# Kernel tuning notes

Measured on AMD Instinct MI355X. Metric: run time of the kernel, lower is better.

The kernel has to match this reference:

```python
import jax, jax.numpy as jnp
import numpy as np

FILTERS = 64
HIDDEN = 128
T_PRED = 24
DILATIONS = (1, 2, 4, 8, 16, 32)
N_DIL = len(DILATIONS)
FEAT = 15
B = 1024
L_ENC = 168


def setup_inputs() -> dict:
    key = jax.random.key(0)
    ks = jax.random.split(key, 16)
    s = 0.05
    d_in = 1 + FEAT  # prev_output (1) concat current feature
    inp = {
        "decoder_features": jax.random.normal(ks[0], (B, T_PRED, FEAT), jnp.float32),
        "decoder_init_input": jax.random.normal(ks[1], (B, 1), jnp.float32),
        "encoder_states": jax.random.normal(ks[2], (N_DIL, B, L_ENC, FILTERS), jnp.float32),
        # dense_1: d_in -> filters (tanh)
        "W1": jax.random.normal(ks[3], (d_in, FILTERS), jnp.float32) * s,
        "b1": jnp.zeros((FILTERS,), jnp.float32),
        # dense_2: filters -> 2*filters (bias)
        "W2": jax.random.normal(ks[4], (FILTERS, 2 * FILTERS), jnp.float32) * s,
        "b2": jnp.zeros((2 * FILTERS,), jnp.float32),
        # dense_3: filters -> 2*filters (no bias)
        "W3": jax.random.normal(ks[5], (FILTERS, 2 * FILTERS), jnp.float32) * s,
        # dense_4: filters -> 2*filters (bias)
        "W4": jax.random.normal(ks[6], (FILTERS, 2 * FILTERS), jnp.float32) * s,
        "b4": jnp.zeros((2 * FILTERS,), jnp.float32),
        # dense_5: n_dil*filters -> hidden (relu)
        "W5": jax.random.normal(ks[7], (N_DIL * FILTERS, HIDDEN), jnp.float32) * s,
        "b5": jnp.zeros((HIDDEN,), jnp.float32),
        # dense_6: hidden -> 1
        "W6": jax.random.normal(ks[8], (HIDDEN, 1), jnp.float32) * s,
        "b6": jnp.zeros((1,), jnp.float32),
    }
    return inp


def _decode(decoder_features, decoder_init_input, encoder_states,
            W1, b1, W2, b2, W3, W4, b4, W5, b5, W6, b6):
    L = encoder_states.shape[2]
    # 'appended' holds the inputs written back into each dilation's state
    # (the growing-concat part of encoder_states in the original loop).
    appended0 = jnp.zeros((N_DIL, decoder_features.shape[0], T_PRED, FILTERS),
                          dtype=decoder_features.dtype)

    def step(carry, t):
        prev, appended = carry
        cur = jnp.concatenate([prev, decoder_features[:, t, :]], axis=1)  # [B, 1+FEAT]
        inputs = jnp.tanh(cur @ W1 + b1)  # [B, F]
        skips_list = []
        for i, d in enumerate(DILATIONS):
            # grown-state read index is (L + t) - d; if t >= d it lands in the
            # appended region (step t-d), otherwise in the original encoder state.
            idx_app = jnp.clip(t - d, 0, T_PRED - 1)
            idx_orig = jnp.clip(L + t - d, 0, L - 1)
            st_app = jax.lax.dynamic_index_in_dim(appended[i], idx_app, axis=1, keepdims=False)
            st_orig = jax.lax.dynamic_index_in_dim(encoder_states[i], idx_orig, axis=1, keepdims=False)
            state = jnp.where(t >= d, st_app, st_orig)  # [B, F]
            dilated = state @ W2 + b2 + inputs @ W3  # [B, 2F]
            conv_filter, conv_gate = dilated[:, :FILTERS], dilated[:, FILTERS:]
            gated = jnp.tanh(conv_filter) * jax.nn.sigmoid(conv_gate)
            out = gated @ W4 + b4  # [B, 2F]
            skips, residuals = out[:, :FILTERS], out[:, FILTERS:]
            inputs = inputs + residuals
            appended = appended.at[i, :, t, :].set(inputs)
            skips_list.append(skips)
        skip = jax.nn.relu(jnp.concatenate(skips_list, axis=1))  # [B, N_DIL*F]
        h = jax.nn.relu(skip @ W5 + b5)
        y = h @ W6 + b6  # [B, 1]
        return (y, appended), y

    (_, _), ys = jax.lax.scan(step, (decoder_init_input, appended0),
                              jnp.arange(T_PRED))
    return jnp.transpose(ys, (1, 0, 2))  # [B, T, 1]


def reference(decoder_features, decoder_init_input, encoder_states,
              W1, b1, W2, b2, W3, W4, b4, W5, b5, W6, b6):
    return _decode(decoder_features, decoder_init_input, encoder_states,
                   W1, b1, W2, b2, W3, W4, b4, W5, b5, W6, b6)
```

## Files before the change

kernel.cpp:

```cpp
#include <hip/hip_runtime.h>

typedef _Float16 h16;
typedef _Float16 half8 __attribute__((ext_vector_type(8)));
typedef float floatx4 __attribute__((ext_vector_type(4)));

#define B_TOT 1024
#define T_STEPS 24
#define F 64
#define C2 128
#define FEAT 15
#define L_ENC 168
#define HID 128
#define R 16
#define BLK 256
#define FP 72
#define W5_WS_ELEMS (12*8*64*8)

__device__ __forceinline__ floatx4 mfma16(half8 a, half8 b, floatx4 c) {
  return __builtin_amdgcn_mfma_f32_16x16x32_f16(a, b, c, 0, 0, 0);
}

__global__ void prep_w5(const float* __restrict__ gW5, h16* __restrict__ wsW5) {
  int t = blockIdx.x * 256 + threadIdx.x;
  if (t >= 12 * 8 * 64) return;
  int lane = t & 63, nt = (t >> 6) & 7, ktg = t >> 9;
  int n  = nt * 16 + (lane & 15);
  int kb = ktg * 32 + (lane >> 4) * 8;
  half8 v;
  #pragma unroll
  for (int j = 0; j < 8; ++j) v[j] = (h16)gW5[(size_t)(kb + j) * C2 + n];
  *(half8*)&wsW5[(size_t)t * 8] = v;
}

__global__ __launch_bounds__(BLK) void decoder_v6(
    const float* __restrict__ dec_feat,
    const float* __restrict__ dec_init,
    const float* __restrict__ enc,
    const float* __restrict__ gW1, const float* __restrict__ gb1,
    const float* __restrict__ gW2, const float* __restrict__ gb2,
    const float* __restrict__ gW3,
    const float* __restrict__ gW4, const float* __restrict__ gb4,
    const h16*  __restrict__ wsW5, const float* __restrict__ gb5,
    const float* __restrict__ gW6, const float* __restrict__ gb6,
    float* __restrict__ out)
{
  __shared__ alignas(16) h16 sW2B[8][2][64][8];
  __shared__ alignas(16) h16 sW3B[8][2][64][8];
  __shared__ alignas(16) h16 sW4B[8][2][64][8];
  __shared__ alignas(16) h16 sW1B[4][64][8];
  __shared__ alignas(16) h16 ringL[31][R][FP];
  __shared__ alignas(16) h16 xH[R][FP];
  __shared__ alignas(16) float x32[R][F];
  __shared__ alignas(16) h16 gatedH[R][FP];
  __shared__ alignas(16) h16 skipH[R][FP];
  __shared__ alignas(16) h16 curH[R][40];
  __shared__ float sb1[F], sb2[C2], sb4[C2], sb5[HID], sW6v[HID];
  __shared__ float ypart[4][R];
  __shared__ float sb6;

  const int tid  = threadIdx.x;
  const int w    = tid >> 6;
  const int lane = tid & 63;
  const int m16  = lane & 15;
  const int q    = lane >> 4;
  const int q8   = q * 8;
  const int b0   = blockIdx.x * R;

  #pragma unroll
  for (int it = 0; it < 4; ++it) {
    int tsk = tid + BLK * it;
    int ln = tsk & 63, kt = (tsk >> 6) & 1, nt = tsk >> 7;
    int n  = nt * 16 + (ln & 15);
    int kb = kt * 32 + (ln >> 4) * 8;
    half8 v2, v3, v4;
    #pragma unroll
    for (int j = 0; j < 8; ++j) {
      v2[j] = (h16)gW2[(kb + j) * C2 + n];
      v3[j] = (h16)gW3[(kb + j) * C2 + n];
      v4[j] = (h16)gW4[(kb + j) * C2 + n];
    }
    *(half8*)&sW2B[nt][kt][ln][0] = v2;
    *(half8*)&sW3B[nt][kt][ln][0] = v3;
    *(half8*)&sW4B[nt][kt][ln][0] = v4;
  }
  {
    int nt = tid >> 6, ln = tid & 63;
    int n  = nt * 16 + (ln & 15);
    int kb = (ln >> 4) * 8;
    half8 v;
    #pragma unroll
    for (int j = 0; j < 8; ++j) {
      int k = kb + j;
      v[j] = (k < 16) ? (h16)gW1[k * F + n] : (h16)0.0f;
    }
    *(half8*)&sW1B[nt][ln][0] = v;
  }
  if (tid < F) sb1[tid] = gb1[tid];
  if (tid < C2) { sb2[tid] = gb2[tid]; sb4[tid] = gb4[tid]; sb5[tid] = gb5[tid]; sW6v[tid] = gW6[tid]; }
  if (tid == 0) sb6 = gb6[0];
  { int mm = tid >> 4, kk = 16 + (tid & 15); curH[mm][kk] = (h16)0.0f; }
  if (tid < R * FEAT) { int mm = tid / FEAT, f = tid % FEAT;
    curH[mm][1 + f] = (h16)dec_feat[(b0 + mm) * (T_STEPS * FEAT) + f]; }
  if (tid < R) curH[tid][0] = (h16)dec_init[b0 + tid];
  __syncthreads();

  const int rbase[6] = {0, 1, 3, 7, 15, 0};

  auto loadStat = [&](half8* dst, int i, int d, int base, int t) {
    if (t >= d) {
      const h16* p = &ringL[base + (t & (d - 1))][m16][0];
      dst[0] = *(const half8*)(p + q8);
      dst[1] = *(const half8*)(p + 32 + q8);
    } else {
      const float* ep = enc + (((size_t)i * B_TOT + b0 + m16) * L_ENC + (L_ENC + t - d)) * F;
      #pragma unroll
      for (int kt = 0; kt < 2; ++kt) {
        float4 e0 = *(const float4*)(ep + kt * 32 + q8);
        float4 e1 = *(const float4*)(ep + kt * 32 + q8 + 4);
        half8 hv;
        hv[0] = (h16)e0.x; hv[1] = (h16)e0.y; hv[2] = (h16)e0.z; hv[3] = (h16)e0.w;
        hv[4] = (h16)e1.x; hv[5] = (h16)e1.y; hv[6] = (h16)e1.z; hv[7] = (h16)e1.w;
        dst[kt] = hv;
      }
    }
  };

  for (int t = 0; t < T_STEPS; ++t) {
    half8 aCur = *(const half8*)&curH[m16][q8];
    half8 bW1  = *(const half8*)&sW1B[w][lane][0];
    floatx4 accX = {0.f, 0.f, 0.f, 0.f};
    accX = mfma16(aCur, bW1, accX);
    half8 stat[2];
    loadStat(stat, 0, 1, rbase[0], t);
    {
      int col = w * 16 + m16;
      #pragma unroll
      for (int j = 0; j < 4; ++j) {
        int row = q * 4 + j;
        float v = tanhf(accX[j] + sb1[col]);
        x32[row][col] = v;
        xH[row][col]  = (h16)v;
      }
    }
    __syncthreads();

    floatx4 hAccA = {0.f, 0.f, 0.f, 0.f};
    floatx4 hAccB = {0.f, 0.f, 0.f, 0.f};

    #pragma unroll
    for (int i = 0; i < 6; ++i) {
      const int d = 1 << i;
      half8 xA0 = *(const half8*)&xH[m16][q8];
      half8 xA1 = *(const half8*)&xH[m16][32 + q8];
      half8 stN[2];
      if (i < 5) loadStat(stN, i + 1, d << 1, rbase[i + 1], t);
      half8 w5f[4];
      #pragma unroll
      for (int kt = 0; kt < 2; ++kt)
        #pragma unroll
        for (int nn = 0; nn < 2; ++nn)
          w5f[kt * 2 + nn] =
              *(const half8*)&wsW5[(size_t)((((2 * i + kt) * 8) + (w + 4 * nn)) * 64 + lane) * 8];

      floatx4 aF = {0.f, 0.f, 0.f, 0.f}, aG = {0.f, 0.f, 0.f, 0.f};
      aF = mfma16(stat[0], *(const half8*)&sW2B[w][0][lane][0], aF);
      aF = mfma16(stat[1], *(const half8*)&sW2B[w][1][lane][0], aF);
      aF = mfma16(xA0,     *(const half8*)&sW3B[w][0][lane][0], aF);
      aF = mfma16(xA1,     *(const half8*)&sW3B[w][1][lane][0], aF);
      aG = mfma16(stat[0], *(const half8*)&sW2B[w + 4][0][lane][0], aG);
      aG = mfma16(stat[1], *(const half8*)&sW2B[w + 4][1][lane][0], aG);
      aG = mfma16(xA0,     *(const half8*)&sW3B[w + 4][0][lane][0], aG);
      aG = mfma16(xA1,     *(const half8*)&sW3B[w + 4][1][lane][0], aG);
      {
        int colF = w * 16 + m16;
        #pragma unroll
        for (int j = 0; j < 4; ++j) {
          int row = q * 4 + j;
          float f = aF[j] + sb2[colF];
          float g = aG[j] + sb2[64 + colF];
          float gt = tanhf(f) / (1.0f + expf(-g));
          gatedH[row][colF] = (h16)gt;
        }
      }
      __syncthreads();

      half8 gA0 = *(const half8*)&gatedH[m16][q8];
      half8 gA1 = *(const half8*)&gatedH[m16][32 + q8];
      floatx4 oS = {0.f, 0.f, 0.f, 0.f}, oR = {0.f, 0.f, 0.f, 0.f};
      oS = mfma16(gA0, *(const half8*)&sW4B[w][0][lane][0], oS);
      oS = mfma16(gA1, *(const half8*)&sW4B[w][1][lane][0], oS);
      oR = mfma16(gA0, *(const half8*)&sW4B[w + 4][0][lane][0], oR);
      oR = mfma16(gA1, *(const half8*)&sW4B[w + 4][1][lane][0], oR);
      {
        int col = w * 16 + m16;
        #pragma unroll
        for (int j = 0; j < 4; ++j) {
          int row = q * 4 + j;
          float s = oS[j] + sb4[col];
          skipH[row][col] = (h16)fmaxf(s, 0.0f);
          float rr = oR[j] + sb4[64 + col];
          float xn = x32[row][col] + rr;
          x32[row][col] = xn;
          h16 hx = (h16)xn;
          xH[row][col] = hx;
          if (i < 5) ringL[rbase[i] + (t & (d - 1))][row][col] = hx;
        }
      }
      __syncthreads();

      half8 sk0 = *(const half8*)&skipH[m16][q8];
      half8 sk1 = *(const half8*)&skipH[m16][32 + q8];
      hAccA = mfma16(sk0, w5f[0], hAccA);
      hAccA = mfma16(sk1, w5f[2], hAccA);
      hAccB = mfma16(sk0, w5f[1], hAccB);
      hAccB = mfma16(sk1, w5f[3], hAccB);

      if (i < 5) { stat[0] = stN[0]; stat[1] = stN[1]; }
    }

    {
      int colA = w * 16 + m16;
      floatx4 vv;
      #pragma unroll
      for (int j = 0; j < 4; ++j) {
        float ha = fmaxf(hAccA[j] + sb5[colA], 0.0f);
        float hb = fmaxf(hAccB[j] + sb5[64 + colA], 0.0f);
        vv[j] = ha * sW6v[colA] + hb * sW6v[64 + colA];
      }
      #pragma unroll
      for (int off = 1; off < 16; off <<= 1) {
        #pragma unroll
        for (int j = 0; j < 4; ++j) vv[j] += __shfl_xor(vv[j], off, 16);
      }
      if (m16 == 0) {
        #pragma unroll
        for (int j = 0; j < 4; ++j) ypart[w][q * 4 + j] = vv[j];
      }
    }
    if (t + 1 < T_STEPS && tid < R * FEAT) {
      int mm = tid / FEAT, f = tid % FEAT;
      curH[mm][1 + f] = (h16)dec_feat[(b0 + mm) * (T_STEPS * FEAT) + (t + 1) * FEAT + f];
    }
    __syncthreads();
    if (tid < R) {
      float y = ypart[0][tid] + ypart[1][tid] + ypart[2][tid] + ypart[3][tid] + sb6;
      out[(b0 + tid) * T_STEPS + t] = y;
      curH[tid][0] = (h16)y;
    }
    __syncthreads();
  }
}

extern "C" void kernel_launch(void* const* d_in, const int* in_sizes, int n_in,
                              void* d_out, int out_size, void* d_ws, size_t ws_size,
                              hipStream_t stream) {
  const float* dec_feat = (const float*)d_in[0];
  const float* dec_init = (const float*)d_in[1];
  const float* enc      = (const float*)d_in[2];
  const float* W1 = (const float*)d_in[3];
  const float* b1 = (const float*)d_in[4];
  const float* W2 = (const float*)d_in[5];
  const float* b2 = (const float*)d_in[6];
  const float* W3 = (const float*)d_in[7];
  const float* W4 = (const float*)d_in[8];
  const float* b4 = (const float*)d_in[9];
  const float* W5 = (const float*)d_in[10];
  const float* b5 = (const float*)d_in[11];
  const float* W6 = (const float*)d_in[12];
  const float* b6 = (const float*)d_in[13];
  float* out = (float*)d_out;
  h16* wsW5 = (h16*)d_ws;

  prep_w5<<<24, 256, 0, stream>>>(W5, wsW5);
  decoder_v6<<<dim3(B_TOT / R), dim3(BLK), 0, stream>>>(
      dec_feat, dec_init, enc, W1, b1, W2, b2, W3, W4, b4, wsW5, b5, W6, b6, out);
}
```

Before: 538.3 us.

## Keep weights and biases in registers, use fast tanh/sigmoid, lighter barriers

```diff
diff --git a/kernel.cpp b/kernel.cpp
--- a/kernel.cpp
+++ b/kernel.cpp
@@ -14,10 +14,24 @@
 #define R 16
 #define BLK 256
 #define FP 72
-#define W5_WS_ELEMS (12*8*64*8)
 
 __device__ __forceinline__ floatx4 mfma16(half8 a, half8 b, floatx4 c) {
   return __builtin_amdgcn_mfma_f32_16x16x32_f16(a, b, c, 0, 0, 0);
+}
+
+#define BAR() asm volatile("s_waitcnt lgkmcnt(0)\n\ts_barrier" ::: "memory")
+
+__device__ __forceinline__ float tanh_fast(float x) {
+  float cx = fminf(fmaxf(x, -15.f), 15.f);
+  float e  = __builtin_amdgcn_exp2f(-2.885390081777927f * cx);
+  return (1.f - e) * __builtin_amdgcn_rcpf(1.f + e);
+}
+__device__ __forceinline__ float gate_fast(float f, float g) {
+  float cf = fminf(fmaxf(f, -15.f), 15.f);
+  float cg = fminf(fmaxf(g, -30.f), 30.f);
+  float ef = __builtin_amdgcn_exp2f(-2.885390081777927f * cf);
+  float eg = __builtin_amdgcn_exp2f(-1.4426950408889634f * cg);
+  return (1.f - ef) * __builtin_amdgcn_rcpf((1.f + ef) * (1.f + eg));
 }
 
 __global__ void prep_w5(const float* __restrict__ gW5, h16* __restrict__ wsW5) {
@@ -32,7 +46,7 @@
   *(half8*)&wsW5[(size_t)t * 8] = v;
 }
 
-__global__ __launch_bounds__(BLK) void decoder_v6(
+__global__ __launch_bounds__(BLK, 1) void decoder_v7(
     const float* __restrict__ dec_feat,
     const float* __restrict__ dec_init,
     const float* __restrict__ enc,
@@ -44,19 +58,12 @@
     const float* __restrict__ gW6, const float* __restrict__ gb6,
     float* __restrict__ out)
 {
-  __shared__ alignas(16) h16 sW2B[8][2][64][8];
-  __shared__ alignas(16) h16 sW3B[8][2][64][8];
-  __shared__ alignas(16) h16 sW4B[8][2][64][8];
-  __shared__ alignas(16) h16 sW1B[4][64][8];
   __shared__ alignas(16) h16 ringL[31][R][FP];
   __shared__ alignas(16) h16 xH[R][FP];
-  __shared__ alignas(16) float x32[R][F];
   __shared__ alignas(16) h16 gatedH[R][FP];
   __shared__ alignas(16) h16 skipH[R][FP];
   __shared__ alignas(16) h16 curH[R][40];
-  __shared__ float sb1[F], sb2[C2], sb4[C2], sb5[HID], sW6v[HID];
   __shared__ float ypart[4][R];
-  __shared__ float sb6;
 
   const int tid  = threadIdx.x;
   const int w    = tid >> 6;
@@ -65,42 +72,53 @@
   const int q    = lane >> 4;
   const int q8   = q * 8;
   const int b0   = blockIdx.x * R;
-
-  #pragma unroll
-  for (int it = 0; it < 4; ++it) {
-    int tsk = tid + BLK * it;
-    int ln = tsk & 63, kt = (tsk >> 6) & 1, nt = tsk >> 7;
-    int n  = nt * 16 + (ln & 15);
-    int kb = kt * 32 + (ln >> 4) * 8;
-    half8 v2, v3, v4;
-    #pragma unroll
-    for (int j = 0; j < 8; ++j) {
-      v2[j] = (h16)gW2[(kb + j) * C2 + n];
-      v3[j] = (h16)gW3[(kb + j) * C2 + n];
-      v4[j] = (h16)gW4[(kb + j) * C2 + n];
-    }
-    *(half8*)&sW2B[nt][kt][ln][0] = v2;
-    *(half8*)&sW3B[nt][kt][ln][0] = v3;
-    *(half8*)&sW4B[nt][kt][ln][0] = v4;
+  const int col  = w * 16 + m16;
+  const int mm0  = tid / FEAT;
+  const int f0   = tid - mm0 * FEAT;
+  const bool featT = (tid < R * FEAT);
+
+  half8 rW1;
+  #pragma unroll
+  for (int j = 0; j < 8; ++j) {
+    int k = q8 + j;
+    rW1[j] = (k < 16) ? (h16)gW1[k * F + col] : (h16)0.0f;
   }
-  {
-    int nt = tid >> 6, ln = tid & 63;
-    int n  = nt * 16 + (ln & 15);
-    int kb = (ln >> 4) * 8;
-    half8 v;
-    #pragma unroll
-    for (int j = 0; j < 8; ++j) {
-      int k = kb + j;
-      v[j] = (k < 16) ? (h16)gW1[k * F + n] : (h16)0.0f;
-    }
-    *(half8*)&sW1B[nt][ln][0] = v;
+  half8 rW2[2][2], rW3[2][2], rW4[2][2];
+  #pragma unroll
+  for (int h = 0; h < 2; ++h) {
+    int n = (w + 4 * h) * 16 + m16;
+    #pragma unroll
+    for (int kt = 0; kt < 2; ++kt) {
+      half8 v2, v3, v4;
+      #pragma unroll
+      for (int j = 0; j < 8; ++j) {
+        int k = kt * 32 + q8 + j;
+        v2[j] = (h16)gW2[k * C2 + n];
+        v3[j] = (h16)gW3[k * C2 + n];
+        v4[j] = (h16)gW4[k * C2 + n];
+      }
+      rW2[h][kt] = v2; rW3[h][kt] = v3; rW4[h][kt] = v4;
+    }
   }
-  if (tid < F) sb1[tid] = gb1[tid];
-  if (tid < C2) { sb2[tid] = gb2[tid]; sb4[tid] = gb4[tid]; sb5[tid] = gb5[tid]; sW6v[tid] = gW6[tid]; }
-  if (tid == 0) sb6 = gb6[0];
+  half8 w5r[6][4];
+  #pragma unroll
+  for (int i = 0; i < 6; ++i)
+    #pragma unroll
+    for (int kt = 0; kt < 2; ++kt)
+      #pragma unroll
+      for (int nn = 0; nn < 2; ++nn)
+        w5r[i][kt * 2 + nn] =
+            *(const half8*)&wsW5[(size_t)((((2 * i + kt) * 8) + (w + 4 * nn)) * 64 + lane) * 8];
+
+  const float rb1  = gb1[col];
+  const float rb2f = gb2[col], rb2g = gb2[64 + col];
+  const float rb4s = gb4[col], rb4r = gb4[64 + col];
+  const float rb5a = gb5[col], rb5b = gb5[64 + col];
+  const float rw6a = gW6[col], rw6b = gW6[64 + col];
+  const float rb6  = gb6[0];
+
   { int mm = tid >> 4, kk = 16 + (tid & 15); curH[mm][kk] = (h16)0.0f; }
-  if (tid < R * FEAT) { int mm = tid / FEAT, f = tid % FEAT;
-    curH[mm][1 + f] = (h16)dec_feat[(b0 + mm) * (T_STEPS * FEAT) + f]; }
+  if (featT) curH[mm0][1 + f0] = (h16)dec_feat[(b0 + mm0) * (T_STEPS * FEAT) + f0];
   if (tid < R) curH[tid][0] = (h16)dec_init[b0 + tid];
   __syncthreads();
 
@@ -125,24 +143,25 @@
     }
   };
 
+  float xr[4];
+
   for (int t = 0; t < T_STEPS; ++t) {
+    float nf = 0.f;
+    const bool doFeat = featT && (t + 1 < T_STEPS);
+    if (doFeat) nf = dec_feat[(b0 + mm0) * (T_STEPS * FEAT) + (t + 1) * FEAT + f0];
+
     half8 aCur = *(const half8*)&curH[m16][q8];
-    half8 bW1  = *(const half8*)&sW1B[w][lane][0];
     floatx4 accX = {0.f, 0.f, 0.f, 0.f};
-    accX = mfma16(aCur, bW1, accX);
+    accX = mfma16(aCur, rW1, accX);
     half8 stat[2];
-    loadStat(stat, 0, 1, rbase[0], t);
-    {
-      int col = w * 16 + m16;
-      #pragma unroll
-      for (int j = 0; j < 4; ++j) {
-        int row = q * 4 + j;
-        float v = tanhf(accX[j] + sb1[col]);
-        x32[row][col] = v;
-        xH[row][col]  = (h16)v;
-      }
-    }
-    __syncthreads();
+    loadStat(stat, 0, 1, 0, t);
+    #pragma unroll
+    for (int j = 0; j < 4; ++j) {
+      float v = tanh_fast(accX[j] + rb1);
+      xr[j] = v;
+      xH[q * 4 + j][col] = (h16)v;
+    }
+    BAR();
 
     floatx4 hAccA = {0.f, 0.f, 0.f, 0.f};
     floatx4 hAccB = {0.f, 0.f, 0.f, 0.f};
@@ -154,78 +173,58 @@
       half8 xA1 = *(const half8*)&xH[m16][32 + q8];
       half8 stN[2];
       if (i < 5) loadStat(stN, i + 1, d << 1, rbase[i + 1], t);
-      half8 w5f[4];
-      #pragma unroll
-      for (int kt = 0; kt < 2; ++kt)
-        #pragma unroll
-        for (int nn = 0; nn < 2; ++nn)
-          w5f[kt * 2 + nn] =
-              *(const half8*)&wsW5[(size_t)((((2 * i + kt) * 8) + (w + 4 * nn)) * 64 + lane) * 8];
 
       floatx4 aF = {0.f, 0.f, 0.f, 0.f}, aG = {0.f, 0.f, 0.f, 0.f};
-      aF = mfma16(stat[0], *(const half8*)&sW2B[w][0][lane][0], aF);
-      aF = mfma16(stat[1], *(const half8*)&sW2B[w][1][lane][0], aF);
-      aF = mfma16(xA0,     *(const half8*)&sW3B[w][0][lane][0], aF);
-      aF = mfma16(xA1,     *(const half8*)&sW3B[w][1][lane][0], aF);
-      aG = mfma16(stat[0], *(const half8*)&sW2B[w + 4][0][lane][0], aG);
-      aG = mfma16(stat[1], *(const half8*)&sW2B[w + 4][1][lane][0], aG);
-      aG = mfma16(xA0,     *(const half8*)&sW3B[w + 4][0][lane][0], aG);
-      aG = mfma16(xA1,     *(const half8*)&sW3B[w + 4][1][lane][0], aG);
-      {
-        int colF = w * 16 + m16;
-        #pragma unroll
-        for (int j = 0; j < 4; ++j) {
-          int row = q * 4 + j;
-          float f = aF[j] + sb2[colF];
-          float g = aG[j] + sb2[64 + colF];
-          float gt = tanhf(f) / (1.0f + expf(-g));
-          gatedH[row][colF] = (h16)gt;
-        }
-      }
-      __syncthreads();
+      aF = mfma16(stat[0], rW2[0][0], aF);
+      aF = mfma16(stat[1], rW2[0][1], aF);
+      aF = mfma16(xA0,     rW3[0][0], aF);
+      aF = mfma16(xA1,     rW3[0][1], aF);
+      aG = mfma16(stat[0], rW2[1][0], aG);
+      aG = mfma16(stat[1], rW2[1][1], aG);
+      aG = mfma16(xA0,     rW3[1][0], aG);
+      aG = mfma16(xA1,     rW3[1][1], aG);
+      #pragma unroll
+      for (int j = 0; j < 4; ++j)
+        gatedH[q * 4 + j][col] = (h16)gate_fast(aF[j] + rb2f, aG[j] + rb2g);
+      BAR();
 
       half8 gA0 = *(const half8*)&gatedH[m16][q8];
       half8 gA1 = *(const half8*)&gatedH[m16][32 + q8];
       floatx4 oS = {0.f, 0.f, 0.f, 0.f}, oR = {0.f, 0.f, 0.f, 0.f};
-      oS = mfma16(gA0, *(const half8*)&sW4B[w][0][lane][0], oS);
-      oS = mfma16(gA1, *(const half8*)&sW4B[w][1][lane][0], oS);
-      oR = mfma16(gA0, *(const half8*)&sW4B[w + 4][0][lane][0], oR);
-      oR = mfma16(gA1, *(const half8*)&sW4B[w + 4][1][lane][0], oR);
-      {
-        int col = w * 16 + m16;
-        #pragma unroll
-        for (int j = 0; j < 4; ++j) {
-          int row = q * 4 + j;
-          float s = oS[j] + sb4[col];
-          skipH[row][col] = (h16)fmaxf(s, 0.0f);
-          float rr = oR[j] + sb4[64 + col];
-          float xn = x32[row][col] + rr;
-          x32[row][col] = xn;
-          h16 hx = (h16)xn;
-          xH[row][col] = hx;
-          if (i < 5) ringL[rbase[i] + (t & (d - 1))][row][col] = hx;
-        }
-      }
-      __syncthreads();
+      oS = mfma16(gA0, rW4[0][0], oS);
+      oS = mfma16(gA1, rW4[0][1], oS);
+      oR = mfma16(gA0, rW4[1][0], oR);
+      oR = mfma16(gA1, rW4[1][1], oR);
+      #pragma unroll
+      for (int j = 0; j < 4; ++j) {
+        int row = q * 4 + j;
+        float s = oS[j] + rb4s;
+        skipH[row][col] = (h16)fmaxf(s, 0.0f);
+        float xn = xr[j] + oR[j] + rb4r;
+        xr[j] = xn;
+        h16 hx = (h16)xn;
+        xH[row][col] = hx;
+        if (i < 5) ringL[rbase[i] + (t & (d - 1))][row][col] = hx;
+      }
+      BAR();
 
       half8 sk0 = *(const half8*)&skipH[m16][q8];
       half8 sk1 = *(const half8*)&skipH[m16][32 + q8];
-      hAccA = mfma16(sk0, w5f[0], hAccA);
-      hAccA = mfma16(sk1, w5f[2], hAccA);
-      hAccB = mfma16(sk0, w5f[1], hAccB);
-      hAccB = mfma16(sk1, w5f[3], hAccB);
+      hAccA = mfma16(sk0, w5r[i][0], hAccA);
+      hAccA = mfma16(sk1, w5r[i][2], hAccA);
+      hAccB = mfma16(sk0, w5r[i][1], hAccB);
+      hAccB = mfma16(sk1, w5r[i][3], hAccB);
 
       if (i < 5) { stat[0] = stN[0]; stat[1] = stN[1]; }
     }
 
     {
-      int colA = w * 16 + m16;
       floatx4 vv;
       #pragma unroll
       for (int j = 0; j < 4; ++j) {
-        float ha = fmaxf(hAccA[j] + sb5[colA], 0.0f);
-        float hb = fmaxf(hAccB[j] + sb5[64 + colA], 0.0f);
-        vv[j] = ha * sW6v[colA] + hb * sW6v[64 + colA];
+        float ha = fmaxf(hAccA[j] + rb5a, 0.0f);
+        float hb = fmaxf(hAccB[j] + rb5b, 0.0f);
+        vv[j] = ha * rw6a + hb * rw6b;
       }
       #pragma unroll
       for (int off = 1; off < 16; off <<= 1) {
@@ -237,17 +236,14 @@
         for (int j = 0; j < 4; ++j) ypart[w][q * 4 + j] = vv[j];
       }
     }
-    if (t + 1 < T_STEPS && tid < R * FEAT) {
-      int mm = tid / FEAT, f = tid % FEAT;
-      curH[mm][1 + f] = (h16)dec_feat[(b0 + mm) * (T_STEPS * FEAT) + (t + 1) * FEAT + f];
-    }
-    __syncthreads();
+    if (doFeat) curH[mm0][1 + f0] = (h16)nf;
+    BAR();
     if (tid < R) {
-      float y = ypart[0][tid] + ypart[1][tid] + ypart[2][tid] + ypart[3][tid] + sb6;
+      float y = ypart[0][tid] + ypart[1][tid] + ypart[2][tid] + ypart[3][tid] + rb6;
       out[(b0 + tid) * T_STEPS + t] = y;
       curH[tid][0] = (h16)y;
     }
-    __syncthreads();
+    BAR();
   }
 }
 
@@ -272,6 +268,6 @@
   h16* wsW5 = (h16*)d_ws;
 
   prep_w5<<<24, 256, 0, stream>>>(W5, wsW5);
-  decoder_v6<<<dim3(B_TOT / R), dim3(BLK), 0, stream>>>(
+  decoder_v7<<<dim3(B_TOT / R), dim3(BLK), 0, stream>>>(
       dec_feat, dec_init, enc, W1, b1, W2, b2, W3, W4, b4, wsW5, b5, W6, b6, out);
 }
```

New measurement: 471.5 us. -12.4%, faster.
